# Kernel optimization log

Measured on AMD Instinct MI355X. Metric: run time of the kernel, lower is better.

Reference implementation:

```python
import jax, jax.numpy as jnp
import numpy as np

N = 50000   # nodes
E = 800000  # edges
F = 256     # input features
H = 256     # hidden units
L = 128     # n_labels
EPS = 1e-5


def setup_inputs():
    key = jax.random.key(0)
    ks = jax.random.split(key, 17)
    s = 0.05
    return {
        "features": jax.random.normal(ks[0], (N, F), jnp.float32),
        "edge_vals": jax.random.uniform(ks[1], (E,), jnp.float32),
        "W1": jax.random.normal(ks[2], (F, H), jnp.float32) * s,
        "db1": jax.random.normal(ks[3], (H,), jnp.float32) * s,
        "b1": jax.random.normal(ks[4], (H,), jnp.float32) * s,
        "g1": jax.random.uniform(ks[5], (H,), jnp.float32, 0.5, 1.5),
        "be1": jax.random.normal(ks[6], (H,), jnp.float32) * s,
        "W2": jax.random.normal(ks[7], (H, H), jnp.float32) * s,
        "b2": jax.random.normal(ks[8], (H,), jnp.float32) * s,
        "g2": jax.random.uniform(ks[9], (H,), jnp.float32, 0.5, 1.5),
        "be2": jax.random.normal(ks[10], (H,), jnp.float32) * s,
        "Wf": jax.random.normal(ks[11], (H, L), jnp.float32) * s,
        "bf": jax.random.normal(ks[12], (L,), jnp.float32) * s,
        "edge_rows": jax.random.randint(ks[13], (E,), 0, N, jnp.int32),
        "edge_cols": jax.random.randint(ks[14], (E,), 0, N, jnp.int32),
        "idx": jax.random.randint(ks[15], (N // 2,), 0, N, jnp.int32),
    }


def _spmm(edge_vals, rows, cols, x):
    # out[i] = sum_{(i,j) in E} A[i,j] * x[j]  (COO sparse @ dense)
    return jax.ops.segment_sum(edge_vals[:, None] * x[cols], rows, num_segments=N)


def _bn(x, gamma, beta):
    # training-mode BatchNormalization: batch (population) stats over nodes
    m = jnp.mean(x, axis=0)
    v = jnp.var(x, axis=0)
    return (x - m) * jax.lax.rsqrt(v + EPS) * gamma + beta


def reference(features, edge_vals, W1, db1, b1, g1, be1, W2, b2, g2, be2, Wf, bf,
              edge_rows, edge_cols, idx):
    # layer 1 (Dense has bias only for l == 0)
    h = features @ W1 + db1
    h = _spmm(edge_vals, edge_rows, edge_cols, h) + b1
    h = jax.nn.relu(_bn(h, g1, be1))
    # layer 2 (no dense bias)
    h = h @ W2
    h = _spmm(edge_vals, edge_rows, edge_cols, h) + b2
    h = jax.nn.relu(_bn(h, g2, be2))
    # dropout = identity (deterministic baseline); final dense head
    out = h @ Wf + bf
    return out[idx]
```

## Files before the change

### kernel.cpp

```cpp
#include <hip/hip_runtime.h>
#include <stdint.h>

#define NN 50000
#define EE 800000
#define FF 256
#define HH 256
#define LL 128
#define SBLK 1024
#define CSRCAP 1200128

typedef __bf16 bf16x8 __attribute__((ext_vector_type(8)));
typedef float  f32x4  __attribute__((ext_vector_type(4)));
typedef unsigned int u32x2 __attribute__((ext_vector_type(2)));
typedef unsigned int u32x4 __attribute__((ext_vector_type(4)));

typedef __attribute__((address_space(1))) unsigned int uint_as1;
typedef __attribute__((address_space(3))) unsigned int uint_as3;

__device__ __forceinline__ unsigned short f2bf(float f) {
  union { float f; unsigned int u; } v; v.f = f;
  unsigned int u = v.u;
  u += 0x7FFFu + ((u >> 16) & 1u);
  return (unsigned short)(u >> 16);
}

__device__ __forceinline__ float bf2f(unsigned short u) {
  union { unsigned int u; float f; } v;
  v.u = ((unsigned int)u) << 16;
  return v.f;
}

__device__ __forceinline__ f32x4 bf4_to_f32(ushort4 u) {
  f32x4 r;
  r.x = bf2f(u.x); r.y = bf2f(u.y); r.z = bf2f(u.z); r.w = bf2f(u.w);
  return r;
}

__device__ __forceinline__ void gload_lds16(const void* g, void* l) {
  __builtin_amdgcn_global_load_lds((const uint_as1*)g, (uint_as3*)l, 16, 0, 0);
}

__global__ __launch_bounds__(256) void k_setup(const int* __restrict__ erows,
                                               int* __restrict__ cnt,
                                               const float* __restrict__ features,
                                               unsigned short* __restrict__ Xb,
                                               const float* __restrict__ W1,
                                               unsigned short* __restrict__ W1t,
                                               const float* __restrict__ W2,
                                               unsigned short* __restrict__ W2t,
                                               const float* __restrict__ Wf,
                                               unsigned short* __restrict__ Wft) {
  __shared__ float tl[64 * 65];
  int b = blockIdx.x, t = threadIdx.x;
  if (b < 3125) {
    int i = b * 256 + t;
    if (i < EE) atomicAdd(&cnt[erows[i]], 1);
  } else if (b < 15625) {
    int i = (b - 3125) * 256 + t;
    f32x4 x = ((const f32x4*)features)[i];
    ushort4 o;
    o.x = f2bf(x.x); o.y = f2bf(x.y); o.z = f2bf(x.z); o.w = f2bf(x.w);
    ((ushort4*)Xb)[i] = o;
  } else {
    int tt = b - 15625;
    const float* in;
    unsigned short* out;
    int Nin, k0, n0;
    if (tt < 16) {
      in = W1; out = W1t; Nin = HH;
      k0 = (tt >> 2) * 64; n0 = (tt & 3) * 64;
    } else if (tt < 32) {
      in = W2; out = W2t; Nin = HH;
      tt -= 16; k0 = (tt >> 2) * 64; n0 = (tt & 3) * 64;
    } else {
      in = Wf; out = Wft; Nin = LL;
      tt -= 32; k0 = (tt >> 1) * 64; n0 = (tt & 1) * 64;
    }
#pragma unroll
    for (int j = 0; j < 16; ++j) {
      int idx = j * 256 + t;
      int r = idx >> 6, c = idx & 63;
      tl[r * 65 + c] = in[(size_t)(k0 + r) * Nin + n0 + c];
    }
    __syncthreads();
#pragma unroll
    for (int j = 0; j < 16; ++j) {
      int idx = j * 256 + t;
      int r = idx >> 6, c = idx & 63;
      out[(size_t)(n0 + r) * HH + k0 + c] = f2bf(tl[c * 65 + r]);
    }
  }
}

__global__ __launch_bounds__(256) void k_alloc(const int* __restrict__ cnt,
                                               int* __restrict__ cursor,
                                               int* __restrict__ total, int n) {
  int i = blockIdx.x * 256 + threadIdx.x;
  int lane = threadIdx.x & 63;
  int c = (i < n) ? ((cnt[i] + 7) & ~7) : 0;
  int incl = c;
#pragma unroll
  for (int off = 1; off < 64; off <<= 1) {
    int v = __shfl_up(incl, off, 64);
    if (lane >= off) incl += v;
  }
  int excl = incl - c;
  int wtot = __shfl(incl, 63, 64);
  int base = 0;
  if (lane == 0) base = atomicAdd(total, wtot);
  base = __shfl(base, 0, 64);
  if (i < n) cursor[i] = base + excl;
}

__global__ __launch_bounds__(256, 3) void k_l1(const unsigned short* __restrict__ A,
                                               const unsigned short* __restrict__ Bt,
                                               const float* __restrict__ bias,
                                               unsigned short* __restrict__ C,
                                               int M, int K, int Nn,
                                               const int* __restrict__ rows,
                                               const int* __restrict__ cols,
                                               const float* __restrict__ vals,
                                               int* __restrict__ cursor,
                                               unsigned int* __restrict__ csr, int E) {
  __shared__ unsigned short lA[128 * 64];
  __shared__ unsigned short lB[128 * 64];
  const int b = blockIdx.x;
  const int tid = threadIdx.x;
  if (b & 1) {
    for (int i = (b >> 1) * 256 + tid; i < E; i += 782 * 256) {
      int p = atomicAdd(&cursor[rows[i]], 1);
      csr[p] = ((unsigned int)cols[i] << 16) | (unsigned int)f2bf(vals[i]);
    }
    return;
  }
  const int gb = b >> 1;
  const int m0 = (gb % 391) * 128, n0 = (gb / 391) * 128;
  const int wave = tid >> 6, lane = tid & 63;
  const int wm = (wave >> 1) * 64, wn = (wave & 1) * 64;
  const int lhi = lane >> 4, llo = lane & 15;
  const int srow = lane >> 3;
  const int scol = (lane & 7) * 8;
  const unsigned short *pA[4], *pB[4];
#pragma unroll
  for (int j = 0; j < 4; ++j) {
    int base = (wave * 4 + j) * 8 + srow;
    int ar = m0 + base;
    ar = ar < M ? ar : 0;
    pA[j] = A + (size_t)ar * K + scol;
    pB[j] = Bt + (size_t)(n0 + base) * K + scol;
  }
  f32x4 zero = {0.f, 0.f, 0.f, 0.f};
  f32x4 acc[4][4];
#pragma unroll
  for (int i = 0; i < 4; ++i)
#pragma unroll
    for (int j = 0; j < 4; ++j) acc[i][j] = zero;
  for (int k0 = 0; k0 < K; k0 += 64) {
#pragma unroll
    for (int j = 0; j < 4; ++j) {
      gload_lds16(pA[j] + k0, lA + (wave * 4 + j) * 8 * 64);
      gload_lds16(pB[j] + k0, lB + (wave * 4 + j) * 8 * 64);
    }
    __syncthreads();
    bf16x8 af[2][4], bfv[2][4];
#pragma unroll
    for (int ks = 0; ks < 2; ++ks) {
#pragma unroll
      for (int mt = 0; mt < 4; ++mt)
        af[ks][mt] = *(const bf16x8*)(lA + (wm + mt * 16 + llo) * 64 + ks * 32 + lhi * 8);
#pragma unroll
      for (int nt = 0; nt < 4; ++nt)
        bfv[ks][nt] = *(const bf16x8*)(lB + (wn + nt * 16 + llo) * 64 + ks * 32 + lhi * 8);
    }
#pragma unroll
    for (int ks = 0; ks < 2; ++ks)
#pragma unroll
      for (int mt = 0; mt < 4; ++mt)
#pragma unroll
        for (int nt = 0; nt < 4; ++nt)
          acc[mt][nt] = __builtin_amdgcn_mfma_f32_16x16x32_bf16(af[ks][mt], bfv[ks][nt], acc[mt][nt], 0, 0, 0);
    __syncthreads();
  }
#pragma unroll
  for (int nt = 0; nt < 4; ++nt) {
    int cn = n0 + wn + nt * 16 + llo;
    float bv = bias[cn];
    unsigned short* Cs = C + (size_t)(cn >> 5) * ((size_t)NN * 32) + (cn & 31);
#pragma unroll
    for (int mt = 0; mt < 4; ++mt) {
      int cm0 = m0 + wm + mt * 16 + lhi * 4;
#pragma unroll
      for (int r = 0; r < 4; ++r) {
        int cm = cm0 + r;
        if (cm < M) Cs[(size_t)cm * 32] = f2bf(acc[mt][nt][r] + bv);
      }
    }
  }
}

__global__ __launch_bounds__(256) void k_spmm(const unsigned short* __restrict__ X,
                                              const int* __restrict__ endp,
                                              const int* __restrict__ cnt,
                                              const unsigned int* __restrict__ csr,
                                              unsigned short* __restrict__ Y, int n) {
  const int slice = blockIdx.x & 7;
  const int S = gridDim.x >> 3;
  const int NRB = (n + 31) >> 5;
  const int wave = threadIdx.x >> 6, lane = threadIdx.x & 63;
  const int grp = lane >> 3;
  const int cl = lane & 7;
  const unsigned short* Xs = X + (size_t)slice * ((size_t)NN * 32) + cl * 4;

  int rb = blockIdx.x >> 3;
  int row = rb * 32 + wave * 8 + grp;
  int q = 0, e = 0;
  if (rb < NRB && row < n) {
    const int c = cnt[row];
    q = endp[row] - c;
    e = q + ((c + 7) & ~7);
  }
  while (rb < NRB) {
    const int rb2 = rb + S;
    const int row2 = rb2 * 32 + wave * 8 + grp;
    int q2 = 0, e2 = 0;
    if (rb2 < NRB && row2 < n) {
      const int c = cnt[row2];
      q2 = endp[row2] - c;
      e2 = q2 + ((c + 7) & ~7);
    }
    f32x4 a0 = {0.f, 0.f, 0.f, 0.f}, a1 = a0, a2 = a0, a3 = a0;
    auto oct = [&](u32x4 ca, u32x4 cb) {
      const ushort4 x0 = *(const ushort4*)(Xs + ((size_t)(ca.x >> 16) << 5));
      const ushort4 x1 = *(const ushort4*)(Xs + ((size_t)(ca.y >> 16) << 5));
      const ushort4 x2 = *(const ushort4*)(Xs + ((size_t)(ca.z >> 16) << 5));
      const ushort4 x3 = *(const ushort4*)(Xs + ((size_t)(ca.w >> 16) << 5));
      const ushort4 x4 = *(const ushort4*)(Xs + ((size_t)(cb.x >> 16) << 5));
      const ushort4 x5 = *(const ushort4*)(Xs + ((size_t)(cb.y >> 16) << 5));
      const ushort4 x6 = *(const ushort4*)(Xs + ((size_t)(cb.z >> 16) << 5));
      const ushort4 x7 = *(const ushort4*)(Xs + ((size_t)(cb.w >> 16) << 5));
      a0 += bf2f((unsigned short)ca.x) * bf4_to_f32(x0);
      a1 += bf2f((unsigned short)ca.y) * bf4_to_f32(x1);
      a2 += bf2f((unsigned short)ca.z) * bf4_to_f32(x2);
      a3 += bf2f((unsigned short)ca.w) * bf4_to_f32(x3);
      a0 += bf2f((unsigned short)cb.x) * bf4_to_f32(x4);
      a1 += bf2f((unsigned short)cb.y) * bf4_to_f32(x5);
      a2 += bf2f((unsigned short)cb.z) * bf4_to_f32(x6);
      a3 += bf2f((unsigned short)cb.w) * bf4_to_f32(x7);
    };
    if (q < e) {
      u32x4 ca = __builtin_nontemporal_load((const u32x4*)(csr + q));
      u32x4 cb = __builtin_nontemporal_load((const u32x4*)(csr + q + 4));
      for (q += 8; q < e; q += 8) {
        u32x4 na = __builtin_nontemporal_load((const u32x4*)(csr + q));
        u32x4 nb = __builtin_nontemporal_load((const u32x4*)(csr + q + 4));
        oct(ca, cb);
        ca = na; cb = nb;
      }
      oct(ca, cb);
    }
    if (row < n) {
      const f32x4 a = (a0 + a1) + (a2 + a3);
      u32x2 o;
      o.x = ((unsigned int)f2bf(a.y) << 16) | (unsigned int)f2bf(a.x);
      o.y = ((unsigned int)f2bf(a.w) << 16) | (unsigned int)f2bf(a.z);
      __builtin_nontemporal_store(o, (u32x2*)(Y + (size_t)row * HH + slice * 32 + cl * 4));
    }
    rb = rb2; row = row2; q = q2; e = e2;
  }
}

__global__ __launch_bounds__(256) void k_bnstats(const unsigned short* __restrict__ X,
                                                 float* __restrict__ part, int n) {
  __shared__ float red[4][64][9];
  const int w = threadIdx.x >> 6, l = threadIdx.x & 63;
  f32x4 s = {0.f, 0.f, 0.f, 0.f}, s2 = {0.f, 0.f, 0.f, 0.f};
  for (int r = blockIdx.x * 4 + w; r < n; r += gridDim.x * 4) {
    f32x4 v = bf4_to_f32(((const ushort4*)(X + (size_t)r * HH))[l]);
    s += v;
    s2 += v * v;
  }
#pragma unroll
  for (int j = 0; j < 4; ++j) { red[w][l][j] = s[j]; red[w][l][4 + j] = s2[j]; }
  __syncthreads();
  if (threadIdx.x < 64) {
    int ll = threadIdx.x;
#pragma unroll
    for (int j = 0; j < 8; ++j) {
      float v = red[0][ll][j] + red[1][ll][j] + red[2][ll][j] + red[3][ll][j];
      int c = ll * 4 + (j & 3);
      part[((j < 4) ? 0 : (SBLK * 256)) + blockIdx.x * 256 + c] = v;
    }
  }
}

__global__ __launch_bounds__(256) void k_bnred(const float* __restrict__ part,
                                               float* __restrict__ sums) {
  int c = threadIdx.x;
  int stat = blockIdx.x >> 3, chunk = blockIdx.x & 7;
  const float* p = part + stat * (SBLK * 256) + chunk * 128 * 256;
  float s0 = 0.f, s1 = 0.f, s2 = 0.f, s3 = 0.f;
  for (int b = 0; b < 128; b += 4) {
    s0 += p[(b + 0) * 256 + c];
    s1 += p[(b + 1) * 256 + c];
    s2 += p[(b + 2) * 256 + c];
    s3 += p[(b + 3) * 256 + c];
  }
  atomicAdd(&sums[stat * HH + c], (s0 + s1) + (s2 + s3));
}

__global__ __launch_bounds__(256) void k_bnrc(const unsigned short* __restrict__ X,
                                              const float* __restrict__ sums,
                                              const float* __restrict__ g,
                                              const float* __restrict__ be,
                                              unsigned short* __restrict__ out, int n4) {
  __shared__ float sc[HH], sh[HH];
  int t = threadIdx.x;
  {
    float inv = 1.f / (float)NN;
    float mean = sums[t] * inv;
    float var = sums[HH + t] * inv - mean * mean;
    float s = g[t] * rsqrtf(var + 1e-5f);
    sc[t] = s;
    sh[t] = be[t] - mean * s;
  }
  __syncthreads();
  for (int i = blockIdx.x * 256 + t; i < n4; i += gridDim.x * 256) {
    f32x4 x = bf4_to_f32(((const ushort4*)X)[i]);
    int c0 = (i * 4) & (HH - 1);
    ushort4 o;
    o.x = f2bf(fmaxf(x.x * sc[c0 + 0] + sh[c0 + 0], 0.f));
    o.y = f2bf(fmaxf(x.y * sc[c0 + 1] + sh[c0 + 1], 0.f));
    o.z = f2bf(fmaxf(x.z * sc[c0 + 2] + sh[c0 + 2], 0.f));
    o.w = f2bf(fmaxf(x.w * sc[c0 + 3] + sh[c0 + 3], 0.f));
    ((ushort4*)out)[i] = o;
  }
}

__global__ __launch_bounds__(256) void k_bnrc_pack(const unsigned short* __restrict__ X,
                                                   const float* __restrict__ sums,
                                                   const float* __restrict__ g,
                                                   const float* __restrict__ be,
                                                   const int* __restrict__ idx,
                                                   unsigned short* __restrict__ out) {
  __shared__ float sc[HH], sh[HH];
  int t = threadIdx.x;
  {
    float inv = 1.f / (float)NN;
    float mean = sums[t] * inv;
    float var = sums[HH + t] * inv - mean * mean;
    float s = g[t] * rsqrtf(var + 1e-5f);
    sc[t] = s;
    sh[t] = be[t] - mean * s;
  }
  __syncthreads();
  int i = blockIdx.x * 256 + t;
  int orow = i >> 6;
  int c0 = (i & 63) * 4;
  int irow = idx[orow];
  f32x4 x = bf4_to_f32(*(const ushort4*)(X + (size_t)irow * HH + c0));
  ushort4 o;
  o.x = f2bf(fmaxf(x.x * sc[c0 + 0] + sh[c0 + 0], 0.f));
  o.y = f2bf(fmaxf(x.y * sc[c0 + 1] + sh[c0 + 1], 0.f));
  o.z = f2bf(fmaxf(x.z * sc[c0 + 2] + sh[c0 + 2], 0.f));
  o.w = f2bf(fmaxf(x.w * sc[c0 + 3] + sh[c0 + 3], 0.f));
  ((ushort4*)out)[i] = o;
}

template <int OUTB>
__global__ __launch_bounds__(256, 3) void k_gemm(const unsigned short* __restrict__ A,
                                                 const unsigned short* __restrict__ Bt,
                                                 const float* __restrict__ bias,
                                                 void* __restrict__ Cv,
                                                 int M, int K, int Nn) {
  __shared__ unsigned short lA[128 * 64];
  __shared__ unsigned short lB[128 * 64];
  const int tid = threadIdx.x;
  const int wave = tid >> 6, lane = tid & 63;
  const int m0 = blockIdx.x * 128, n0 = blockIdx.y * 128;
  const int wm = (wave >> 1) * 64, wn = (wave & 1) * 64;
  const int lhi = lane >> 4, llo = lane & 15;
  const int srow = lane >> 3;
  const int scol = (lane & 7) * 8;
  const unsigned short *pA[4], *pB[4];
#pragma unroll
  for (int j = 0; j < 4; ++j) {
    int base = (wave * 4 + j) * 8 + srow;
    int ar = m0 + base;
    ar = ar < M ? ar : 0;
    pA[j] = A + (size_t)ar * K + scol;
    pB[j] = Bt + (size_t)(n0 + base) * K + scol;
  }
  f32x4 zero = {0.f, 0.f, 0.f, 0.f};
  f32x4 acc[4][4];
#pragma unroll
  for (int i = 0; i < 4; ++i)
#pragma unroll
    for (int j = 0; j < 4; ++j) acc[i][j] = zero;
  for (int k0 = 0; k0 < K; k0 += 64) {
#pragma unroll
    for (int j = 0; j < 4; ++j) {
      gload_lds16(pA[j] + k0, lA + (wave * 4 + j) * 8 * 64);
      gload_lds16(pB[j] + k0, lB + (wave * 4 + j) * 8 * 64);
    }
    __syncthreads();
    bf16x8 af[2][4], bfv[2][4];
#pragma unroll
    for (int ks = 0; ks < 2; ++ks) {
#pragma unroll
      for (int mt = 0; mt < 4; ++mt)
        af[ks][mt] = *(const bf16x8*)(lA + (wm + mt * 16 + llo) * 64 + ks * 32 + lhi * 8);
#pragma unroll
      for (int nt = 0; nt < 4; ++nt)
        bfv[ks][nt] = *(const bf16x8*)(lB + (wn + nt * 16 + llo) * 64 + ks * 32 + lhi * 8);
    }
#pragma unroll
    for (int ks = 0; ks < 2; ++ks)
#pragma unroll
      for (int mt = 0; mt < 4; ++mt)
#pragma unroll
        for (int nt = 0; nt < 4; ++nt)
          acc[mt][nt] = __builtin_amdgcn_mfma_f32_16x16x32_bf16(af[ks][mt], bfv[ks][nt], acc[mt][nt], 0, 0, 0);
    __syncthreads();
  }
#pragma unroll
  for (int nt = 0; nt < 4; ++nt) {
    int cn = n0 + wn + nt * 16 + llo;
    float bv = bias ? bias[cn] : 0.f;
#pragma unroll
    for (int mt = 0; mt < 4; ++mt) {
      int cm0 = m0 + wm + mt * 16 + lhi * 4;
#pragma unroll
      for (int r = 0; r < 4; ++r) {
        int cm = cm0 + r;
        if (cm < M) {
          float v = acc[mt][nt][r] + bv;
          if (OUTB)
            ((unsigned short*)Cv)[(size_t)(cn >> 5) * ((size_t)NN * 32) +
                                  (size_t)cm * 32 + (cn & 31)] = f2bf(v);
          else
            ((float*)Cv)[(size_t)cm * Nn + cn] = v;
        }
      }
    }
  }
}

extern "C" void kernel_launch(void* const* d_in, const int* in_sizes, int n_in,
                              void* d_out, int out_size, void* d_ws, size_t ws_size,
                              hipStream_t stream) {
  const float* features = (const float*)d_in[0];
  const float* edge_vals = (const float*)d_in[1];
  const float* W1 = (const float*)d_in[2];
  const float* db1 = (const float*)d_in[3];
  const float* g1 = (const float*)d_in[5];
  const float* be1 = (const float*)d_in[6];
  const float* W2 = (const float*)d_in[7];
  const float* g2 = (const float*)d_in[9];
  const float* be2 = (const float*)d_in[10];
  const float* Wf = (const float*)d_in[11];
  const float* bfb = (const float*)d_in[12];
  const int* erows = (const int*)d_in[13];
  const int* ecols = (const int*)d_in[14];
  const int* idx = (const int*)d_in[15];
  const int M3 = in_sizes[15];
  (void)n_in; (void)out_size; (void)ws_size;

  char* ws = (char*)d_ws;
  size_t off = 0;
  auto alloc = [&](size_t bytes) -> void* {
    void* p = (void*)(ws + off);
    off += (bytes + 255) & ~(size_t)255;
    return p;
  };
  unsigned short* Xb = (unsigned short*)alloc((size_t)NN * HH * 2);
  unsigned short* Ab = (unsigned short*)alloc((size_t)NN * HH * 2);
  unsigned short* Yb = (unsigned short*)alloc((size_t)NN * HH * 2);
  unsigned short* Pb = (unsigned short*)alloc((size_t)25000 * HH * 2);
  unsigned short* W1t = (unsigned short*)alloc((size_t)FF * HH * 2);
  unsigned short* W2t = (unsigned short*)alloc((size_t)HH * HH * 2);
  unsigned short* Wft = (unsigned short*)alloc((size_t)HH * LL * 2);
  int* cursor = (int*)alloc((size_t)NN * 4);
  int* cnt = (int*)alloc((size_t)NN * 4);
  unsigned int* csr = (unsigned int*)alloc((size_t)CSRCAP * 4);
  float* part = (float*)alloc((size_t)2 * SBLK * 256 * 4);
  float* stats = (float*)alloc(4 * HH * 4 + 256);
  float* sums1 = stats;
  float* sums2 = stats + 2 * HH;
  int* total = (int*)(stats + 4 * HH);

  hipMemsetAsync(cnt, 0, (size_t)NN * 4, stream);
  hipMemsetAsync(csr, 0, (size_t)CSRCAP * 4, stream);
  hipMemsetAsync(stats, 0, 4 * HH * 4 + 256, stream);

  k_setup<<<15665, 256, 0, stream>>>(erows, cnt, features, Xb, W1, W1t, W2, W2t, Wf, Wft);
  k_alloc<<<(NN + 255) / 256, 256, 0, stream>>>(cnt, cursor, total, NN);

  k_l1<<<1564, 256, 0, stream>>>(Xb, W1t, db1, Ab, NN, FF, HH,
                                 erows, ecols, edge_vals, cursor, csr, EE);
  k_spmm<<<8 * 391, 256, 0, stream>>>(Ab, cursor, cnt, csr, Yb, NN);
  k_bnstats<<<SBLK, 256, 0, stream>>>(Yb, part, NN);
  k_bnred<<<16, 256, 0, stream>>>(part, sums1);
  k_bnrc<<<2048, 256, 0, stream>>>(Yb, sums1, g1, be1, Xb, NN * HH / 4);

  k_gemm<1><<<dim3((NN + 127) / 128, HH / 128), 256, 0, stream>>>(Xb, W2t, nullptr, Ab, NN, HH, HH);
  k_spmm<<<8 * 391, 256, 0, stream>>>(Ab, cursor, cnt, csr, Yb, NN);
  k_bnstats<<<SBLK, 256, 0, stream>>>(Yb, part, NN);
  k_bnred<<<16, 256, 0, stream>>>(part, sums2);
  k_bnrc_pack<<<(M3 * 64) / 256, 256, 0, stream>>>(Yb, sums2, g2, be2, idx, Pb);

  k_gemm<0><<<dim3((M3 + 127) / 128, LL / 128), 256, 0, stream>>>(Pb, Wft, bfb, d_out, M3, HH, LL);
}
```

Baseline: 501.3 us.

## Stage per-block CSR segment in LDS and launch one block per row group

```diff
diff --git a/kernel.cpp b/kernel.cpp
--- a/kernel.cpp
+++ b/kernel.cpp
@@ -8,6 +8,7 @@
 #define LL 128
 #define SBLK 1024
 #define CSRCAP 1200128
+#define SCAP 4096
 
 typedef __bf16 bf16x8 __attribute__((ext_vector_type(8)));
 typedef float  f32x4  __attribute__((ext_vector_type(4)));
@@ -203,54 +204,64 @@
                                               const int* __restrict__ cnt,
                                               const unsigned int* __restrict__ csr,
                                               unsigned short* __restrict__ Y, int n) {
+  __shared__ unsigned int lcsr[SCAP];
   const int slice = blockIdx.x & 7;
-  const int S = gridDim.x >> 3;
-  const int NRB = (n + 31) >> 5;
-  const int wave = threadIdx.x >> 6, lane = threadIdx.x & 63;
+  const int r0 = (blockIdx.x >> 3) * 32;
+  const int tid = threadIdx.x;
+  const int wave = tid >> 6, lane = tid & 63;
   const int grp = lane >> 3;
   const int cl = lane & 7;
   const unsigned short* Xs = X + (size_t)slice * ((size_t)NN * 32) + cl * 4;
 
-  int rb = blockIdx.x >> 3;
-  int row = rb * 32 + wave * 8 + grp;
-  int q = 0, e = 0;
-  if (rb < NRB && row < n) {
-    const int c = cnt[row];
-    q = endp[row] - c;
-    e = q + ((c + 7) & ~7);
-  }
-  while (rb < NRB) {
-    const int rb2 = rb + S;
-    const int row2 = rb2 * 32 + wave * 8 + grp;
-    int q2 = 0, e2 = 0;
-    if (rb2 < NRB && row2 < n) {
-      const int c = cnt[row2];
-      q2 = endp[row2] - c;
-      e2 = q2 + ((c + 7) & ~7);
-    }
-    f32x4 a0 = {0.f, 0.f, 0.f, 0.f}, a1 = a0, a2 = a0, a3 = a0;
-    auto oct = [&](u32x4 ca, u32x4 cb) {
-      const ushort4 x0 = *(const ushort4*)(Xs + ((size_t)(ca.x >> 16) << 5));
-      const ushort4 x1 = *(const ushort4*)(Xs + ((size_t)(ca.y >> 16) << 5));
-      const ushort4 x2 = *(const ushort4*)(Xs + ((size_t)(ca.z >> 16) << 5));
-      const ushort4 x3 = *(const ushort4*)(Xs + ((size_t)(ca.w >> 16) << 5));
-      const ushort4 x4 = *(const ushort4*)(Xs + ((size_t)(cb.x >> 16) << 5));
-      const ushort4 x5 = *(const ushort4*)(Xs + ((size_t)(cb.y >> 16) << 5));
-      const ushort4 x6 = *(const ushort4*)(Xs + ((size_t)(cb.z >> 16) << 5));
-      const ushort4 x7 = *(const ushort4*)(Xs + ((size_t)(cb.w >> 16) << 5));
-      a0 += bf2f((unsigned short)ca.x) * bf4_to_f32(x0);
-      a1 += bf2f((unsigned short)ca.y) * bf4_to_f32(x1);
-      a2 += bf2f((unsigned short)ca.z) * bf4_to_f32(x2);
-      a3 += bf2f((unsigned short)ca.w) * bf4_to_f32(x3);
-      a0 += bf2f((unsigned short)cb.x) * bf4_to_f32(x4);
-      a1 += bf2f((unsigned short)cb.y) * bf4_to_f32(x5);
-      a2 += bf2f((unsigned short)cb.z) * bf4_to_f32(x6);
-      a3 += bf2f((unsigned short)cb.w) * bf4_to_f32(x7);
-    };
-    if (q < e) {
+  const int rlast = (r0 + 31 < n) ? (r0 + 31) : (n - 1);
+  const int s0 = endp[r0] - cnt[r0];
+  const int clast = cnt[rlast];
+  const int send = (endp[rlast] - clast) + ((clast + 7) & ~7);
+  const int len0 = send - s0;
+  const int len = len0 < SCAP ? len0 : SCAP;
+  for (int j = tid * 4; j < len; j += 1024)
+    *(u32x4*)(lcsr + j) = __builtin_nontemporal_load((const u32x4*)(csr + s0 + j));
+  __syncthreads();
+
+  const int row = r0 + wave * 8 + grp;
+  if (row >= n) return;
+  const int c = cnt[row];
+  int q = endp[row] - c;
+  const int qe = q + ((c + 7) & ~7);
+
+  f32x4 a0 = {0.f, 0.f, 0.f, 0.f}, a1 = a0, a2 = a0, a3 = a0;
+  auto oct = [&](u32x4 ca, u32x4 cb) {
+    const ushort4 x0 = *(const ushort4*)(Xs + ((size_t)(ca.x >> 16) << 5));
+    const ushort4 x1 = *(const ushort4*)(Xs + ((size_t)(ca.y >> 16) << 5));
+    const ushort4 x2 = *(const ushort4*)(Xs + ((size_t)(ca.z >> 16) << 5));
+    const ushort4 x3 = *(const ushort4*)(Xs + ((size_t)(ca.w >> 16) << 5));
+    const ushort4 x4 = *(const ushort4*)(Xs + ((size_t)(cb.x >> 16) << 5));
+    const ushort4 x5 = *(const ushort4*)(Xs + ((size_t)(cb.y >> 16) << 5));
+    const ushort4 x6 = *(const ushort4*)(Xs + ((size_t)(cb.z >> 16) << 5));
+    const ushort4 x7 = *(const ushort4*)(Xs + ((size_t)(cb.w >> 16) << 5));
+    a0 += bf2f((unsigned short)ca.x) * bf4_to_f32(x0);
+    a1 += bf2f((unsigned short)ca.y) * bf4_to_f32(x1);
+    a2 += bf2f((unsigned short)ca.z) * bf4_to_f32(x2);
+    a3 += bf2f((unsigned short)ca.w) * bf4_to_f32(x3);
+    a0 += bf2f((unsigned short)cb.x) * bf4_to_f32(x4);
+    a1 += bf2f((unsigned short)cb.y) * bf4_to_f32(x5);
+    a2 += bf2f((unsigned short)cb.z) * bf4_to_f32(x6);
+    a3 += bf2f((unsigned short)cb.w) * bf4_to_f32(x7);
+  };
+
+  if (send - s0 <= len) {
+    const unsigned int* lp = lcsr + (q - s0);
+#pragma unroll 2
+    for (; q < qe; q += 8, lp += 8) {
+      u32x4 ca = *(const u32x4*)(lp);
+      u32x4 cb = *(const u32x4*)(lp + 4);
+      oct(ca, cb);
+    }
+  } else {
+    if (q < qe) {
       u32x4 ca = __builtin_nontemporal_load((const u32x4*)(csr + q));
       u32x4 cb = __builtin_nontemporal_load((const u32x4*)(csr + q + 4));
-      for (q += 8; q < e; q += 8) {
+      for (q += 8; q < qe; q += 8) {
         u32x4 na = __builtin_nontemporal_load((const u32x4*)(csr + q));
         u32x4 nb = __builtin_nontemporal_load((const u32x4*)(csr + q + 4));
         oct(ca, cb);
@@ -258,15 +269,13 @@
       }
       oct(ca, cb);
     }
-    if (row < n) {
-      const f32x4 a = (a0 + a1) + (a2 + a3);
-      u32x2 o;
-      o.x = ((unsigned int)f2bf(a.y) << 16) | (unsigned int)f2bf(a.x);
-      o.y = ((unsigned int)f2bf(a.w) << 16) | (unsigned int)f2bf(a.z);
-      __builtin_nontemporal_store(o, (u32x2*)(Y + (size_t)row * HH + slice * 32 + cl * 4));
-    }
-    rb = rb2; row = row2; q = q2; e = e2;
-  }
+  }
+
+  const f32x4 a = (a0 + a1) + (a2 + a3);
+  u32x2 o;
+  o.x = ((unsigned int)f2bf(a.y) << 16) | (unsigned int)f2bf(a.x);
+  o.y = ((unsigned int)f2bf(a.w) << 16) | (unsigned int)f2bf(a.z);
+  __builtin_nontemporal_store(o, (u32x2*)(Y + (size_t)row * HH + slice * 32 + cl * 4));
 }
 
 __global__ __launch_bounds__(256) void k_bnstats(const unsigned short* __restrict__ X,
@@ -497,13 +506,13 @@
 
   k_l1<<<1564, 256, 0, stream>>>(Xb, W1t, db1, Ab, NN, FF, HH,
                                  erows, ecols, edge_vals, cursor, csr, EE);
-  k_spmm<<<8 * 391, 256, 0, stream>>>(Ab, cursor, cnt, csr, Yb, NN);
+  k_spmm<<<8 * 1563, 256, 0, stream>>>(Ab, cursor, cnt, csr, Yb, NN);
   k_bnstats<<<SBLK, 256, 0, stream>>>(Yb, part, NN);
   k_bnred<<<16, 256, 0, stream>>>(part, sums1);
   k_bnrc<<<2048, 256, 0, stream>>>(Yb, sums1, g1, be1, Xb, NN * HH / 4);
 
   k_gemm<1><<<dim3((NN + 127) / 128, HH / 128), 256, 0, stream>>>(Xb, W2t, nullptr, Ab, NN, HH, HH);
-  k_spmm<<<8 * 391, 256, 0, stream>>>(Ab, cursor, cnt, csr, Yb, NN);
+  k_spmm<<<8 * 1563, 256, 0, stream>>>(Ab, cursor, cnt, csr, Yb, NN);
   k_bnstats<<<SBLK, 256, 0, stream>>>(Yb, part, NN);
   k_bnred<<<16, 256, 0, stream>>>(part, sums2);
   k_bnrc_pack<<<(M3 * 64) / 256, 256, 0, stream>>>(Yb, sums2, g2, be2, idx, Pb);
```

Result: faster. 451.6 us (-9.9%).
